# Kernel tuning notes

Measured on AMD Instinct MI355X. Metric: run time of the kernel, lower is better.

## Reference

```python
import jax, jax.numpy as jnp
import numpy as np

HID = 4096      # hidden_size
H = 32          # num_attention_heads
K = 8           # num_key_value_heads
D = HID // H    # head_dim = 128
G = H // K      # q heads per kv group = 4
INTER = 14336   # intermediate_size
T = 2048        # tokens (prefill)
EPS = 1e-5
THETA = 1000000.0


def setup_inputs() -> dict:
    key = jax.random.key(0)
    ks = jax.random.split(key, 9)
    s = 0.02
    return {
        "hidden_states": jax.random.normal(ks[0], (T, HID), jnp.float32),
        "position_ids": jnp.arange(T, dtype=jnp.int64),
        "wqkv": jax.random.normal(ks[1], ((H + 2 * K) * D, HID), jnp.float32) * s,
        "wo": jax.random.normal(ks[2], (HID, HID), jnp.float32) * s,
        "w1": jax.random.normal(ks[3], (INTER, HID), jnp.float32) * s,  # gate
        "w3": jax.random.normal(ks[4], (INTER, HID), jnp.float32) * s,  # up
        "w2": jax.random.normal(ks[5], (HID, INTER), jnp.float32) * s,  # down
        "attn_norm_w": jnp.ones((HID,), jnp.float32),
        "ffn_norm_w": jnp.ones((HID,), jnp.float32),
    }


def _rmsnorm(x, w):
    var = jnp.mean(jnp.square(x), axis=-1, keepdims=True)
    return x * jax.lax.rsqrt(var + EPS) * w


def _rope(x, cos, sin):
    # non-interleaved (half-split) rotation; x: [T, h, D], cos/sin: [T, 1, D//2]
    x1, x2 = x[..., : D // 2], x[..., D // 2 :]
    return jnp.concatenate([x1 * cos - x2 * sin, x2 * cos + x1 * sin], axis=-1)


def _attention(x, position_ids, wqkv, wo):
    t = x.shape[0]
    qkv = x @ wqkv.T  # [T, (H+2K)*D]
    q = qkv[:, : H * D].reshape(t, H, D)
    k = qkv[:, H * D : (H + K) * D].reshape(t, K, D)
    v = qkv[:, (H + K) * D :].reshape(t, K, D)

    inv_freq = 1.0 / (THETA ** (jnp.arange(0, D, 2, dtype=jnp.float32) / D))
    freqs = position_ids.astype(jnp.float32)[:, None] * inv_freq  # [T, D//2]
    cos = jnp.cos(freqs)[:, None, :]
    sin = jnp.sin(freqs)[:, None, :]
    q = _rope(q, cos, sin)
    k = _rope(k, cos, sin)

    # grouped-query attention: [T, K, G, D] queries vs [T, K, D] keys
    qg = q.reshape(t, K, G, D)
    scale = 1.0 / jnp.sqrt(jnp.float32(D))
    scores = jnp.einsum("tkgd,skd->kgts", qg, k) * scale  # [K, G, T, T]
    causal = jnp.tril(jnp.ones((t, t), dtype=bool))
    scores = jnp.where(causal, scores, jnp.finfo(scores.dtype).min)
    probs = jax.nn.softmax(scores, axis=-1)
    out = jnp.einsum("kgts,skd->tkgd", probs, v).reshape(t, H * D)
    return out @ wo.T


def _mlp(x, w1, w3, w2):
    return (jax.nn.silu(x @ w1.T) * (x @ w3.T)) @ w2.T


def reference(hidden_states, position_ids, wqkv, wo, w1, w3, w2, attn_norm_w, ffn_norm_w):
    h = hidden_states + _attention(_rmsnorm(hidden_states, attn_norm_w), position_ids, wqkv, wo)
    return h + _mlp(_rmsnorm(h, ffn_norm_w), w1, w3, w2)
```

## Files before the change

### kernel.cpp

```cpp
#include <hip/hip_runtime.h>
#include <stdint.h>

#define T_SEQ 2048
#define HIDN  4096
#define NH    32
#define NKV   8
#define DH    128
#define INTER 14336
#define QKV_N 6144
#define EPSR  1e-5f
#define SCALE 0.08838834764831845f
#define KVB   64

typedef __bf16 bf16x8 __attribute__((ext_vector_type(8)));
typedef float  f32x4  __attribute__((ext_vector_type(4)));

__device__ __forceinline__ f32x4 mfma16(bf16x8 a, bf16x8 b, f32x4 c) {
  return __builtin_amdgcn_mfma_f32_16x16x32_bf16(a, b, c, 0, 0, 0);
}

__device__ __forceinline__ void glds16(const void* g, void* l) {
  __builtin_amdgcn_global_load_lds(
      (__attribute__((address_space(1))) void*)g,
      (__attribute__((address_space(3))) void*)l,
      16, 0, 0);
}

__global__ __launch_bounds__(256) void cvt_bf16_kernel(
    const float* __restrict__ src, __bf16* __restrict__ dst, long n) {
  long stride = (long)gridDim.x * 256 * 8;
  for (long i = ((long)blockIdx.x * 256 + threadIdx.x) * 8; i < n; i += stride) {
    float4 a = *(const float4*)(src + i);
    float4 b = *(const float4*)(src + i + 4);
    bf16x8 o;
    o[0]=(__bf16)a.x; o[1]=(__bf16)a.y; o[2]=(__bf16)a.z; o[3]=(__bf16)a.w;
    o[4]=(__bf16)b.x; o[5]=(__bf16)b.y; o[6]=(__bf16)b.z; o[7]=(__bf16)b.w;
    *(bf16x8*)(dst + i) = o;
  }
}

__global__ __launch_bounds__(256) void cvt_w13_kernel(
    const float* __restrict__ w1, const float* __restrict__ w3,
    __bf16* __restrict__ dst) {
  for (int c = blockIdx.x; c < 2 * INTER; c += gridDim.x) {
    int tau = c >> 8, j2 = c & 255;
    int wn = j2 >> 6, j = j2 & 63, nt = j >> 4, k16 = j & 15;
    const float* src = (nt < 2 ? w1 : w3) +
        (size_t)(tau * 128 + wn * 32 + (nt & 1) * 16 + k16) * HIDN;
    __bf16* d = dst + (size_t)c * HIDN;
    int i = threadIdx.x * 16;
    float4 a = *(const float4*)(src + i);
    float4 b = *(const float4*)(src + i + 4);
    float4 e = *(const float4*)(src + i + 8);
    float4 f = *(const float4*)(src + i + 12);
    bf16x8 o0, o1;
    o0[0]=(__bf16)a.x; o0[1]=(__bf16)a.y; o0[2]=(__bf16)a.z; o0[3]=(__bf16)a.w;
    o0[4]=(__bf16)b.x; o0[5]=(__bf16)b.y; o0[6]=(__bf16)b.z; o0[7]=(__bf16)b.w;
    o1[0]=(__bf16)e.x; o1[1]=(__bf16)e.y; o1[2]=(__bf16)e.z; o1[3]=(__bf16)e.w;
    o1[4]=(__bf16)f.x; o1[5]=(__bf16)f.y; o1[6]=(__bf16)f.z; o1[7]=(__bf16)f.w;
    *(bf16x8*)(d + i) = o0;
    *(bf16x8*)(d + i + 8) = o1;
  }
}

__global__ __launch_bounds__(256) void rmsnorm_kernel(
    const float* __restrict__ x, const float* __restrict__ w,
    __bf16* __restrict__ y) {
  const int row = blockIdx.x, tid = threadIdx.x;
  const float* xr = x + (size_t)row * HIDN + tid * 16;
  float4 v0 = ((const float4*)xr)[0];
  float4 v1 = ((const float4*)xr)[1];
  float4 v2 = ((const float4*)xr)[2];
  float4 v3 = ((const float4*)xr)[3];
  float ss = v0.x*v0.x + v0.y*v0.y + v0.z*v0.z + v0.w*v0.w
           + v1.x*v1.x + v1.y*v1.y + v1.z*v1.z + v1.w*v1.w
           + v2.x*v2.x + v2.y*v2.y + v2.z*v2.z + v2.w*v2.w
           + v3.x*v3.x + v3.y*v3.y + v3.z*v3.z + v3.w*v3.w;
  #pragma unroll
  for (int off = 32; off >= 1; off >>= 1) ss += __shfl_xor(ss, off, 64);
  __shared__ float red[4];
  if ((tid & 63) == 0) red[tid >> 6] = ss;
  __syncthreads();
  float rn = rsqrtf((red[0] + red[1] + red[2] + red[3]) * (1.0f / HIDN) + EPSR);
  const float* wr = w + tid * 16;
  #pragma unroll
  for (int h = 0; h < 2; h++) {
    float4 a = ((const float4*)xr)[h*2], b = ((const float4*)xr)[h*2+1];
    float4 wa = ((const float4*)wr)[h*2], wb = ((const float4*)wr)[h*2+1];
    bf16x8 o;
    o[0]=(__bf16)(a.x*rn*wa.x); o[1]=(__bf16)(a.y*rn*wa.y);
    o[2]=(__bf16)(a.z*rn*wa.z); o[3]=(__bf16)(a.w*rn*wa.w);
    o[4]=(__bf16)(b.x*rn*wb.x); o[5]=(__bf16)(b.y*rn*wb.y);
    o[6]=(__bf16)(b.z*rn*wb.z); o[7]=(__bf16)(b.w*rn*wb.w);
    *(bf16x8*)(y + (size_t)row * HIDN + tid * 16 + h * 8) = o;
  }
}

__global__ __launch_bounds__(256) void add3_rms_kernel(
    const float* __restrict__ p, const float* __restrict__ resid,
    const float* __restrict__ w, float* __restrict__ hout,
    __bf16* __restrict__ xn) {
  const int row = blockIdx.x, tid = threadIdx.x;
  const size_t base = (size_t)row * HIDN + tid * 16;
  const size_t half = (size_t)T_SEQ * HIDN;
  float h[16];
  float ss = 0.f;
  #pragma unroll
  for (int q = 0; q < 4; q++) {
    float4 a = *(const float4*)(p + base + q * 4);
    float4 b = *(const float4*)(p + half + base + q * 4);
    float4 c = *(const float4*)(resid + base + q * 4);
    h[q*4+0] = a.x + b.x + c.x; h[q*4+1] = a.y + b.y + c.y;
    h[q*4+2] = a.z + b.z + c.z; h[q*4+3] = a.w + b.w + c.w;
    ss += h[q*4]*h[q*4] + h[q*4+1]*h[q*4+1] + h[q*4+2]*h[q*4+2] + h[q*4+3]*h[q*4+3];
    *(float4*)(hout + base + q * 4) = *(float4*)&h[q*4];
  }
  #pragma unroll
  for (int off = 32; off >= 1; off >>= 1) ss += __shfl_xor(ss, off, 64);
  __shared__ float red[4];
  if ((tid & 63) == 0) red[tid >> 6] = ss;
  __syncthreads();
  float rn = rsqrtf((red[0] + red[1] + red[2] + red[3]) * (1.0f / HIDN) + EPSR);
  #pragma unroll
  for (int hb = 0; hb < 2; hb++) {
    bf16x8 o;
    #pragma unroll
    for (int e = 0; e < 8; e++) {
      float wv = w[tid * 16 + hb * 8 + e];
      o[e] = (__bf16)(h[hb*8+e] * rn * wv);
    }
    *(bf16x8*)(xn + base + hb * 8) = o;
  }
}

template<int EPI>
__global__ __launch_bounds__(512, 2) void gemm256_kernel(
    const __bf16* __restrict__ A, const __bf16* __restrict__ B,
    void* __restrict__ Cout, int M, int N, int Kfull, int KZ, int Nout) {
  extern __shared__ __align__(16) char smem[];
  const int tid = threadIdx.x;
  const int lane = tid & 63;
  const int wv = tid >> 6;
  const int wm = wv >> 2;
  const int wn = wv & 3;
  const int lr = lane & 15, ql = lane >> 4;

  const int gx = gridDim.x, gy = gridDim.y;
  const int nwg = gx * gy;
  const int orig = blockIdx.y * gx + blockIdx.x;
  const int cpx = nwg >> 3;
  const int swz = (orig & 7) * cpx + (orig >> 3);
  const int by = swz % gy, bx = swz / gy;
  const int m0 = by * 256, n0 = bx * 256;
  const int kbase = blockIdx.z * KZ;
  const int NT = KZ >> 6;

  const int u0 = tid, u1 = tid + 512;
  const int r0 = u0 >> 2, r1 = u1 >> 2;
  const int p0 = (u0 & 3) ^ ((r0 >> 1) & 3);
  const int p1 = (u1 & 3) ^ ((r1 >> 1) & 3);
  const char* aR0 = (const char*)(A + (size_t)(m0 + r0) * Kfull + kbase) + p0 * 16;
  const char* aR1 = (const char*)(A + (size_t)(m0 + r1) * Kfull + kbase) + p1 * 16;
  const char* bR0 = (const char*)(B + (size_t)(n0 + r0) * Kfull + kbase) + p0 * 16;
  const char* bR1 = (const char*)(B + (size_t)(n0 + r1) * Kfull + kbase) + p1 * 16;
  const int d0 = u0 * 16, d1 = u1 * 16;

  const int sA = ql ^ ((lr >> 1) & 3);
  int aoff[8], boff[4];
  #pragma unroll
  for (int mt = 0; mt < 8; mt++) aoff[mt] = (wm * 128 + mt * 16 + lr) * 64 + sA * 16;
  #pragma unroll
  for (int nt = 0; nt < 4; nt++) boff[nt] = (wn * 64 + nt * 16 + lr) * 64 + sA * 16;

#define STAGE_A(t, kh, b) do {                                         \
    const size_t _o = (size_t)(t) * 128 + (kh) * 64;                   \
    glds16(aR0 + _o, smem + (b) * 65536 + (kh) * 16384 + d0);          \
    glds16(aR1 + _o, smem + (b) * 65536 + (kh) * 16384 + d1);          \
  } while (0)
#define STAGE_B(t, kh, b) do {                                         \
    const size_t _o = (size_t)(t) * 128 + (kh) * 64;                   \
    glds16(bR0 + _o, smem + (b) * 65536 + 32768 + (kh) * 16384 + d0);  \
    glds16(bR1 + _o, smem + (b) * 65536 + 32768 + (kh) * 16384 + d1);  \
  } while (0)
#define LDA4(dst, mb, b, ks) do {                                      \
    const char* _p = smem + (b) * 65536 + (ks) * 16384;                \
    dst[0] = *(const bf16x8*)(_p + aoff[(mb) + 0]);                    \
    dst[1] = *(const bf16x8*)(_p + aoff[(mb) + 1]);                    \
    dst[2] = *(const bf16x8*)(_p + aoff[(mb) + 2]);                    \
    dst[3] = *(const bf16x8*)(_p + aoff[(mb) + 3]);                    \
  } while (0)
#define LDB4(b, ks) do {                                               \
    const char* _p = smem + (b) * 65536 + 32768 + (ks) * 16384;        \
    bfr[0] = *(const bf16x8*)(_p + boff[0]);                           \
    bfr[1] = *(const bf16x8*)(_p + boff[1]);                           \
    bfr[2] = *(const bf16x8*)(_p + boff[2]);                           \
    bfr[3] = *(const bf16x8*)(_p + boff[3]);                           \
  } while (0)
#define VMW8() asm volatile("s_waitcnt vmcnt(8)" ::: "memory")
#define BAR()  __builtin_amdgcn_s_barrier()
#define WAITK() do { asm volatile("s_waitcnt lgkmcnt(0)" ::: "memory"); \
    __builtin_amdgcn_sched_barrier(0); } while (0)
#define MFMA16(mb, AF) do {                                            \
    __builtin_amdgcn_s_setprio(1);                                     \
    _Pragma("unroll") for (int _m = 0; _m < 4; _m++)                   \
      _Pragma("unroll") for (int _n = 0; _n < 4; _n++)                 \
        acc[(mb) + _m][_n] = mfma16(AF[_m], bfr[_n], acc[(mb) + _m][_n]); \
    __builtin_amdgcn_s_setprio(0);                                     \
  } while (0)

  f32x4 acc[8][4] = {};
  bf16x8 afA[4], afB[4], bfr[4];

  STAGE_A(0, 0, 0); STAGE_B(0, 0, 0);
  STAGE_A(0, 1, 0); STAGE_B(0, 1, 0);
  STAGE_A(1, 0, 1); STAGE_B(1, 0, 1);
  VMW8();
  BAR();

  const int NI = NT >> 1;
  for (int i = 0; i < NI; ++i) {
    const int t1 = 2 * i + 1;
    const int s2 = (2 * i + 2 < NT) ? 2 * i + 2 : NT - 1;
    const int s3 = (2 * i + 3 < NT) ? 2 * i + 3 : NT - 1;
    LDA4(afA, 0, 0, 0); LDB4(0, 0);
    STAGE_A(t1, 1, 1);
    BAR(); WAITK(); MFMA16(0, afA); BAR();
    LDA4(afB, 4, 0, 0);
    STAGE_B(t1, 1, 1);
    VMW8(); BAR(); WAITK(); MFMA16(4, afB); BAR();
    LDA4(afA, 0, 0, 1); LDB4(0, 1);
    STAGE_A(s2, 0, 0);
    BAR(); WAITK(); MFMA16(0, afA); BAR();
    LDA4(afB, 4, 0, 1);
    STAGE_B(s2, 0, 0);
    VMW8(); BAR(); WAITK(); MFMA16(4, afB); BAR();
    LDA4(afA, 0, 1, 0); LDB4(1, 0);
    STAGE_A(s2, 1, 0);
    BAR(); WAITK(); MFMA16(0, afA); BAR();
    LDA4(afB, 4, 1, 0);
    STAGE_B(s2, 1, 0);
    VMW8(); BAR(); WAITK(); MFMA16(4, afB); BAR();
    LDA4(afA, 0, 1, 1); LDB4(1, 1);
    STAGE_A(s3, 0, 1);
    BAR(); WAITK(); MFMA16(0, afA); BAR();
    LDA4(afB, 4, 1, 1);
    STAGE_B(s3, 0, 1);
    VMW8(); BAR(); WAITK(); MFMA16(4, afB); BAR();
  }
  asm volatile("s_waitcnt vmcnt(0)" ::: "memory");

#undef STAGE_A
#undef STAGE_B
#undef LDA4
#undef LDB4
#undef VMW8
#undef BAR
#undef WAITK
#undef MFMA16

  #pragma unroll
  for (int mt = 0; mt < 8; mt++) {
    #pragma unroll
    for (int r = 0; r < 4; r++) {
      int rr = m0 + wm * 128 + mt * 16 + ql * 4 + r;
      if (EPI == 2) {
        #pragma unroll
        for (int nt = 0; nt < 2; nt++) {
          float u = acc[mt][nt][r];
          float v = acc[mt][nt + 2][r];
          float g = u / (1.0f + __expf(-u)) * v;
          int cc = (n0 >> 1) + wn * 32 + nt * 16 + lr;
          ((__bf16*)Cout)[(size_t)rr * Nout + cc] = (__bf16)g;
        }
      } else {
        #pragma unroll
        for (int nt = 0; nt < 4; nt++) {
          int cc = n0 + wn * 64 + nt * 16 + lr;
          size_t ix = (size_t)rr * N + cc;
          float val = acc[mt][nt][r];
          if (EPI == 0) ((float*)Cout)[(size_t)blockIdx.z * M * N + ix] = val;
          else          ((__bf16*)Cout)[ix] = (__bf16)val;
        }
      }
    }
  }
}

__global__ __launch_bounds__(256) void add3_kernel(
    const float* __restrict__ p, const float* __restrict__ r,
    float* __restrict__ o, long n) {
  long stride = (long)gridDim.x * 1024;
  for (long i = ((long)blockIdx.x * 256 + threadIdx.x) * 4; i < n; i += stride) {
    float4 a = *(const float4*)(p + i);
    float4 b = *(const float4*)(p + n + i);
    float4 c = *(const float4*)(r + i);
    float4 o4;
    o4.x = a.x + b.x + c.x; o4.y = a.y + b.y + c.y;
    o4.z = a.z + b.z + c.z; o4.w = a.w + b.w + c.w;
    *(float4*)(o + i) = o4;
  }
}

__global__ __launch_bounds__(256) void rope_kernel(
    const __bf16* __restrict__ qkv, __bf16* __restrict__ q_r,
    __bf16* __restrict__ k_r) {
  const int t = blockIdx.x, tid = threadIdx.x;
  __shared__ float cs[64], sn[64];
  if (tid < 64) {
    float inv = exp2f(-(float)tid * (19.931568569324174f / 64.0f));
    float f = (float)t * inv;
    cs[tid] = cosf(f);
    sn[tid] = sinf(f);
  }
  __syncthreads();
  const __bf16* row = qkv + (size_t)t * QKV_N;
  for (int it = tid; it < 40 * 64; it += 256) {
    int hh = it >> 6, i = it & 63;
    float x1 = (float)row[hh * 128 + i];
    float x2 = (float)row[hh * 128 + 64 + i];
    float c = cs[i], s = sn[i];
    float o1 = x1 * c - x2 * s;
    float o2 = x2 * c + x1 * s;
    if (hh < NH) {
      __bf16* qo = q_r + (size_t)t * HIDN + hh * 128;
      qo[i] = (__bf16)o1;
      qo[64 + i] = (__bf16)o2;
    } else {
      __bf16* ko = k_r + (size_t)t * (NKV * DH) + (hh - NH) * 128;
      ko[i] = (__bf16)o1;
      ko[64 + i] = (__bf16)o2;
    }
  }
}

__global__ __launch_bounds__(256) void vtrans_kernel(
    const __bf16* __restrict__ qkv, __bf16* __restrict__ v_t) {
  __shared__ __bf16 tile[64][136];
  const int tid = threadIdx.x;
  const int t0 = blockIdx.x * 64, kh = blockIdx.y;
  #pragma unroll
  for (int i = 0; i < 4; i++) {
    int u = i * 256 + tid;
    int row = u >> 4, c = (u & 15) * 8;
    *(bf16x8*)&tile[row][c] =
        *(const bf16x8*)(qkv + (size_t)(t0 + row) * QKV_N + (NH + NKV) * DH + kh * DH + c);
  }
  __syncthreads();
  const int d = tid & 127, th = (tid >> 7) * 32;
  #pragma unroll
  for (int j = 0; j < 4; j++) {
    int t = th + j * 8;
    bf16x8 o;
    #pragma unroll
    for (int e = 0; e < 8; e++) o[e] = tile[t + e][d];
    *(bf16x8*)(v_t + ((size_t)kh * DH + d) * T_SEQ + t0 + t) = o;
  }
}

__global__ __launch_bounds__(256) void attn_kernel(
    const __bf16* __restrict__ q_r, const __bf16* __restrict__ k_r,
    const __bf16* __restrict__ v_t, __bf16* __restrict__ attn_o) {
  __shared__ __align__(16) __bf16 Ks[KVB * 128];
  __shared__ __align__(16) __bf16 Vs[128 * KVB];
  __shared__ __align__(16) __bf16 Pl[4 * 16 * KVB];

  const int tid = threadIdx.x;
  const int lane = tid & 63, wv = tid >> 6;
  const int lr = lane & 15, g = lane >> 4;
  const int qt = gridDim.x - 1 - blockIdx.x;
  const int h = blockIdx.y;
  const int kh = h >> 2;
  const int q0b = qt * 64;
  const int q0w = q0b + wv * 16;

  bf16x8 qf[4];
  {
    const __bf16* qp = q_r + (size_t)(q0w + lr) * HIDN + h * DH + g * 8;
    #pragma unroll
    for (int kk = 0; kk < 4; kk++) qf[kk] = *(const bf16x8*)(qp + kk * 32);
  }

  f32x4 o[8] = {};
  float mrun[4] = {-1e30f, -1e30f, -1e30f, -1e30f};
  float lrun[4] = {0.f, 0.f, 0.f, 0.f};
  char* PlW = (char*)Pl + wv * 2048;

  for (int kv0 = 0; kv0 < q0b + KVB; kv0 += KVB) {
    __syncthreads();
    #pragma unroll
    for (int i = 0; i < 4; i++) {
      int u = i * 256 + tid;
      int row = u >> 4;
      int cb = ((u & 15) * 16) ^ ((row & 7) << 4);
      glds16((const char*)(k_r + (size_t)(kv0 + row) * (NKV * DH) + kh * DH) + cb,
             (char*)Ks + u * 16);
    }
    #pragma unroll
    for (int i = 0; i < 4; i++) {
      int u = i * 256 + tid;
      int row = u >> 3;
      int cb = ((u & 7) * 16) ^ ((row & 7) << 4);
      glds16((const char*)(v_t + ((size_t)kh * DH + row) * T_SEQ + kv0) + cb,
             (char*)Vs + u * 16);
    }
    __syncthreads();

    if (q0w + 15 >= kv0) {
      f32x4 s[4] = {};
      #pragma unroll
      for (int kk = 0; kk < 4; kk++) {
        #pragma unroll
        for (int jt = 0; jt < 4; jt++) {
          int krow = jt * 16 + lr;
          int cb = (kk * 64 + g * 16) ^ ((krow & 7) << 4);
          bf16x8 kf = *(const bf16x8*)((char*)Ks + krow * 256 + cb);
          s[jt] = mfma16(qf[kk], kf, s[jt]);
        }
      }
      const bool need_mask = (kv0 + KVB - 1) > q0w;
      #pragma unroll
      for (int r = 0; r < 4; r++) {
        int qpos = q0w + g * 4 + r;
        int prow = g * 4 + r;
        float p[4];
        #pragma unroll
        for (int jt = 0; jt < 4; jt++) {
          float v = s[jt][r] * SCALE;
          if (need_mask && (kv0 + jt * 16 + lr > qpos)) v = -1e30f;
          p[jt] = v;
        }
        float mx = fmaxf(fmaxf(p[0], p[1]), fmaxf(p[2], p[3]));
        #pragma unroll
        for (int off = 1; off < 16; off <<= 1) mx = fmaxf(mx, __shfl_xor(mx, off, 64));
        float mn = fmaxf(mrun[r], mx);
        float corr = __expf(mrun[r] - mn);
        mrun[r] = mn;
        float ps = 0.f;
        #pragma unroll
        for (int jt = 0; jt < 4; jt++) {
          p[jt] = __expf(p[jt] - mn);
          ps += p[jt];
          int cbyte = ((jt * 16 + lr) * 2) ^ ((prow & 7) << 4);
          *(__bf16*)(PlW + prow * 128 + cbyte) = (__bf16)p[jt];
        }
        #pragma unroll
        for (int off = 1; off < 16; off <<= 1) ps += __shfl_xor(ps, off, 64);
        lrun[r] = lrun[r] * corr + ps;
        #pragma unroll
        for (int nt = 0; nt < 8; nt++) o[nt][r] *= corr;
      }
      bf16x8 pa[2];
      #pragma unroll
      for (int ks = 0; ks < 2; ks++)
        pa[ks] = *(const bf16x8*)(PlW + lr * 128 + ((g * 16 + ks * 64) ^ ((lr & 7) << 4)));
      #pragma unroll
      for (int nt = 0; nt < 8; nt++) {
        #pragma unroll
        for (int ks = 0; ks < 2; ks++) {
          int vrow = nt * 16 + lr;
          int cb = (ks * 64 + g * 16) ^ ((vrow & 7) << 4);
          bf16x8 vf = *(const bf16x8*)((char*)Vs + vrow * 128 + cb);
          o[nt] = mfma16(pa[ks], vf, o[nt]);
        }
      }
    }
  }

  #pragma unroll
  for (int nt = 0; nt < 8; nt++) {
    #pragma unroll
    for (int r = 0; r < 4; r++) {
      int qrow = q0w + g * 4 + r;
      int d = nt * 16 + lr;
      attn_o[(size_t)qrow * HIDN + h * DH + d] = (__bf16)(o[nt][r] / lrun[r]);
    }
  }
}

extern "C" void kernel_launch(void* const* d_in, const int* in_sizes, int n_in,
                              void* d_out, int out_size, void* d_ws, size_t ws_size,
                              hipStream_t stream) {
  const float* hidden = (const float*)d_in[0];
  const float* wqkv = (const float*)d_in[2];
  const float* wo   = (const float*)d_in[3];
  const float* w1   = (const float*)d_in[4];
  const float* w3   = (const float*)d_in[5];
  const float* w2   = (const float*)d_in[6];
  const float* anw  = (const float*)d_in[7];
  const float* fnw  = (const float*)d_in[8];

  char* ws = (char*)d_ws;
  const size_t SZ_XN   = (size_t)T_SEQ * HIDN * 2;
  const size_t SZ_QKV  = (size_t)T_SEQ * QKV_N * 2;
  const size_t SZ_KR   = (size_t)T_SEQ * NKV * DH * 2;
  const size_t SZ_H    = (size_t)T_SEQ * HIDN * 4;
  const size_t SZ_UV   = (size_t)T_SEQ * INTER * 2;

  const size_t W_QKV = (size_t)QKV_N * HIDN * 2;
  const size_t W_O   = (size_t)HIDN * HIDN * 2;
  const size_t W_I   = (size_t)INTER * HIDN * 2;
  const size_t W_TOTAL = W_QKV + W_O + 3 * W_I;

  char* act = ws + W_TOTAL;

  __bf16* xn1    = (__bf16*)(act);
  __bf16* qkv    = (__bf16*)(act + SZ_XN);
  __bf16* q_r    = (__bf16*)(act + SZ_XN + SZ_QKV);
  __bf16* gbuf   = (__bf16*)(act);
  __bf16* k_r    = (__bf16*)(act + SZ_UV);
  __bf16* attn_o = (__bf16*)(act + SZ_UV + SZ_KR);
  float*  hbuf   = (float*) (act + SZ_UV + SZ_KR + SZ_XN);
  __bf16* v_t    = (__bf16*)(act + SZ_UV + SZ_KR + SZ_XN);
  __bf16* xn2    = (__bf16*)(act + SZ_UV + SZ_KR + SZ_XN + SZ_H);
  float*  pbuf   = (float*)(act + SZ_UV + SZ_KR + SZ_XN + SZ_H + SZ_XN);

  __bf16* wqkv_b = (__bf16*)(ws);
  __bf16* wo_b   = (__bf16*)(ws + W_QKV);
  __bf16* w13_b  = (__bf16*)(ws + W_QKV + W_O);
  __bf16* w2_b   = (__bf16*)(ws + W_QKV + W_O + 2 * W_I);

  const int LDS_BYTES = 131072;
  hipFuncSetAttribute((const void*)gemm256_kernel<0>,
                      hipFuncAttributeMaxDynamicSharedMemorySize, LDS_BYTES);
  hipFuncSetAttribute((const void*)gemm256_kernel<1>,
                      hipFuncAttributeMaxDynamicSharedMemorySize, LDS_BYTES);
  hipFuncSetAttribute((const void*)gemm256_kernel<2>,
                      hipFuncAttributeMaxDynamicSharedMemorySize, LDS_BYTES);

  cvt_bf16_kernel<<<2048, 256, 0, stream>>>(wqkv, wqkv_b, (long)QKV_N * HIDN);
  cvt_bf16_kernel<<<2048, 256, 0, stream>>>(wo,   wo_b,   (long)HIDN * HIDN);
  cvt_w13_kernel<<<2048, 256, 0, stream>>>(w1, w3, w13_b);
  cvt_bf16_kernel<<<2048, 256, 0, stream>>>(w2,   w2_b,   (long)HIDN * INTER);

  rmsnorm_kernel<<<T_SEQ, 256, 0, stream>>>(hidden, anw, xn1);
  gemm256_kernel<1><<<dim3(QKV_N / 256, T_SEQ / 256, 1), 512, LDS_BYTES, stream>>>(
      xn1, wqkv_b, qkv, T_SEQ, QKV_N, HIDN, HIDN, QKV_N);
  rope_kernel<<<T_SEQ, 256, 0, stream>>>(qkv, q_r, k_r);
  vtrans_kernel<<<dim3(T_SEQ / 64, NKV), 256, 0, stream>>>(qkv, v_t);
  attn_kernel<<<dim3(T_SEQ / 64, NH), 256, 0, stream>>>(q_r, k_r, v_t, attn_o);
  gemm256_kernel<0><<<dim3(HIDN / 256, T_SEQ / 256, 2), 512, LDS_BYTES, stream>>>(
      attn_o, wo_b, pbuf, T_SEQ, HIDN, HIDN, HIDN / 2, HIDN);
  add3_rms_kernel<<<T_SEQ, 256, 0, stream>>>(pbuf, hidden, fnw, hbuf, xn2);
  gemm256_kernel<2><<<dim3(2 * INTER / 256, T_SEQ / 256, 1), 512, LDS_BYTES, stream>>>(
      xn2, w13_b, gbuf, T_SEQ, 2 * INTER, HIDN, HIDN, INTER);
  gemm256_kernel<0><<<dim3(HIDN / 256, T_SEQ / 256, 2), 512, LDS_BYTES, stream>>>(
      gbuf, w2_b, pbuf, T_SEQ, HIDN, INTER, INTER / 2, HIDN);
  add3_kernel<<<2048, 256, 0, stream>>>(pbuf, hbuf, (float*)d_out, (long)T_SEQ * HIDN);
}
```

Baseline: 1.290 ms.

## Software-pipeline LDS fragment loads with MFMA using double-buffered registers

Reworks the GEMM main loop so the LDS reads for the next MFMA group are issued before the current group's MFMAs, using two register sets each for A and B fragments. The full lgkmcnt(0) wait and the barrier pair around each MFMA block become partial lgkmcnt waits and a single barrier per step. The last iteration is peeled into an epilogue that drains the vmcnt counters. This aims to hide LDS latency behind matrix math, at the cost of more VGPRs and tight dependence on exact waitcnt counts.

New measurement: 1.280 ms. Within noise of the previous version (-0.8%).

```diff
diff --git a/kernel.cpp b/kernel.cpp
--- a/kernel.cpp
+++ b/kernel.cpp
@@ -189,73 +189,122 @@
     dst[2] = *(const bf16x8*)(_p + aoff[(mb) + 2]);                    \
     dst[3] = *(const bf16x8*)(_p + aoff[(mb) + 3]);                    \
   } while (0)
-#define LDB4(b, ks) do {                                               \
+#define LDB4(dst, b, ks) do {                                          \
     const char* _p = smem + (b) * 65536 + 32768 + (ks) * 16384;        \
-    bfr[0] = *(const bf16x8*)(_p + boff[0]);                           \
-    bfr[1] = *(const bf16x8*)(_p + boff[1]);                           \
-    bfr[2] = *(const bf16x8*)(_p + boff[2]);                           \
-    bfr[3] = *(const bf16x8*)(_p + boff[3]);                           \
+    dst[0] = *(const bf16x8*)(_p + boff[0]);                           \
+    dst[1] = *(const bf16x8*)(_p + boff[1]);                           \
+    dst[2] = *(const bf16x8*)(_p + boff[2]);                           \
+    dst[3] = *(const bf16x8*)(_p + boff[3]);                           \
   } while (0)
-#define VMW8() asm volatile("s_waitcnt vmcnt(8)" ::: "memory")
-#define BAR()  __builtin_amdgcn_s_barrier()
-#define WAITK() do { asm volatile("s_waitcnt lgkmcnt(0)" ::: "memory"); \
+#define VMW(n)  asm volatile("s_waitcnt vmcnt(" #n ")" ::: "memory")
+#define BAR()   __builtin_amdgcn_s_barrier()
+#define LGKM(n) do { asm volatile("s_waitcnt lgkmcnt(" #n ")" ::: "memory"); \
     __builtin_amdgcn_sched_barrier(0); } while (0)
-#define MFMA16(mb, AF) do {                                            \
+#define MFMA16(mb, AF, BF) do {                                        \
     __builtin_amdgcn_s_setprio(1);                                     \
     _Pragma("unroll") for (int _m = 0; _m < 4; _m++)                   \
       _Pragma("unroll") for (int _n = 0; _n < 4; _n++)                 \
-        acc[(mb) + _m][_n] = mfma16(AF[_m], bfr[_n], acc[(mb) + _m][_n]); \
+        acc[(mb) + _m][_n] = mfma16(AF[_m], BF[_n], acc[(mb) + _m][_n]); \
     __builtin_amdgcn_s_setprio(0);                                     \
   } while (0)
 
   f32x4 acc[8][4] = {};
-  bf16x8 afA[4], afB[4], bfr[4];
+  bf16x8 af0[4], af1[4], bf0[4], bf1[4];
 
   STAGE_A(0, 0, 0); STAGE_B(0, 0, 0);
   STAGE_A(0, 1, 0); STAGE_B(0, 1, 0);
   STAGE_A(1, 0, 1); STAGE_B(1, 0, 1);
-  VMW8();
+  VMW(8);
   BAR();
+  LDA4(af0, 0, 0, 0); LDB4(bf0, 0, 0);
 
   const int NI = NT >> 1;
-  for (int i = 0; i < NI; ++i) {
-    const int t1 = 2 * i + 1;
-    const int s2 = (2 * i + 2 < NT) ? 2 * i + 2 : NT - 1;
-    const int s3 = (2 * i + 3 < NT) ? 2 * i + 3 : NT - 1;
-    LDA4(afA, 0, 0, 0); LDB4(0, 0);
+  for (int i = 0; i < NI - 1; ++i) {
+    const int t1 = 2 * i + 1, s2 = 2 * i + 2, s3 = 2 * i + 3;
+    LDA4(af1, 4, 0, 0);
     STAGE_A(t1, 1, 1);
-    BAR(); WAITK(); MFMA16(0, afA); BAR();
-    LDA4(afB, 4, 0, 0);
+    LGKM(4);
+    MFMA16(0, af0, bf0);
+    VMW(6); BAR();
+    LDA4(af0, 0, 0, 1); LDB4(bf1, 0, 1);
     STAGE_B(t1, 1, 1);
-    VMW8(); BAR(); WAITK(); MFMA16(4, afB); BAR();
-    LDA4(afA, 0, 0, 1); LDB4(0, 1);
+    LGKM(8);
+    MFMA16(4, af1, bf0);
+    VMW(6); BAR();
+    LDA4(af1, 4, 0, 1);
     STAGE_A(s2, 0, 0);
-    BAR(); WAITK(); MFMA16(0, afA); BAR();
-    LDA4(afB, 4, 0, 1);
+    LGKM(4);
+    MFMA16(0, af0, bf1);
+    VMW(6); BAR();
+    LDA4(af0, 0, 1, 0); LDB4(bf0, 1, 0);
     STAGE_B(s2, 0, 0);
-    VMW8(); BAR(); WAITK(); MFMA16(4, afB); BAR();
-    LDA4(afA, 0, 1, 0); LDB4(1, 0);
+    LGKM(8);
+    MFMA16(4, af1, bf1);
+    VMW(6); BAR();
+    LDA4(af1, 4, 1, 0);
     STAGE_A(s2, 1, 0);
-    BAR(); WAITK(); MFMA16(0, afA); BAR();
-    LDA4(afB, 4, 1, 0);
+    LGKM(4);
+    MFMA16(0, af0, bf0);
+    VMW(6); BAR();
+    LDA4(af0, 0, 1, 1); LDB4(bf1, 1, 1);
     STAGE_B(s2, 1, 0);
-    VMW8(); BAR(); WAITK(); MFMA16(4, afB); BAR();
-    LDA4(afA, 0, 1, 1); LDB4(1, 1);
+    LGKM(8);
+    MFMA16(4, af1, bf0);
+    VMW(6); BAR();
+    LDA4(af1, 4, 1, 1);
     STAGE_A(s3, 0, 1);
-    BAR(); WAITK(); MFMA16(0, afA); BAR();
-    LDA4(afB, 4, 1, 1);
+    LGKM(4);
+    MFMA16(0, af0, bf1);
+    VMW(6); BAR();
+    LDA4(af0, 0, 0, 0); LDB4(bf0, 0, 0);
     STAGE_B(s3, 0, 1);
-    VMW8(); BAR(); WAITK(); MFMA16(4, afB); BAR();
-  }
-  asm volatile("s_waitcnt vmcnt(0)" ::: "memory");
+    LGKM(8);
+    MFMA16(4, af1, bf1);
+    VMW(6); BAR();
+  }
+  {
+    const int t1 = NT - 1;
+    LDA4(af1, 4, 0, 0);
+    STAGE_A(t1, 1, 1);
+    LGKM(4);
+    MFMA16(0, af0, bf0);
+    VMW(6); BAR();
+    LDA4(af0, 0, 0, 1); LDB4(bf1, 0, 1);
+    STAGE_B(t1, 1, 1);
+    LGKM(8);
+    MFMA16(4, af1, bf0);
+    BAR();
+    LDA4(af1, 4, 0, 1);
+    LGKM(4);
+    MFMA16(0, af0, bf1);
+    VMW(2); BAR();
+    LDA4(af0, 0, 1, 0); LDB4(bf0, 1, 0);
+    LGKM(8);
+    MFMA16(4, af1, bf1);
+    BAR();
+    LDA4(af1, 4, 1, 0);
+    LGKM(4);
+    MFMA16(0, af0, bf0);
+    VMW(0); BAR();
+    LDA4(af0, 0, 1, 1); LDB4(bf1, 1, 1);
+    LGKM(8);
+    MFMA16(4, af1, bf0);
+    BAR();
+    LDA4(af1, 4, 1, 1);
+    LGKM(4);
+    MFMA16(0, af0, bf1);
+    BAR();
+    LGKM(0);
+    MFMA16(4, af1, bf1);
+  }
 
 #undef STAGE_A
 #undef STAGE_B
 #undef LDA4
 #undef LDB4
-#undef VMW8
+#undef VMW
 #undef BAR
-#undef WAITK
+#undef LGKM
 #undef MFMA16
 
   #pragma unroll
```
